# Kernel tuning notes

Measured on AMD Instinct MI355X. Metric: run time of the kernel, lower is better.

Reference implementation:

```python
import jax, jax.numpy as jnp
import numpy as np

CLP_K = 9
SCL_KS = (3, 4, 3)  # scl0_k, scl1_k, scl2_k from the source


def _ste(f, x):
    # straight-through estimator: forward f(x), identity gradient
    return x + jax.lax.stop_gradient(f(x) - x)


def floor_ste(x):
    return _ste(jnp.floor, x)


def round_ste(x):
    return _ste(jnp.round, x)


def conv_t(x, w, b):
    # torch F.conv_transpose2d with kernel 5, stride 2, padding 2, output_padding 1
    # expressed as an lhs-dilated conv; w is torch layout [in, out, kh, kw]
    k = w.shape[-1]
    wc = jnp.flip(w, axis=(-2, -1)).transpose(1, 0, 2, 3)  # -> [out, in, kh, kw]
    lo = k - 1 - 2           # k-1-padding = 2
    hi = k - 1 - 2 + 1       # + output_padding = 3
    y = jax.lax.conv_general_dilated(
        x, wc, window_strides=(1, 1), padding=[(lo, hi), (lo, hi)],
        lhs_dilation=(2, 2), dimension_numbers=('NCHW', 'OIHW', 'NCHW'))
    return y + b[None, :, None, None]


def split_deconv(x, w, b, split):
    # sum of `split` transposed convs with floor((round(W)+j)/split) quantized weights
    out = 0.0
    for j in range(split):
        wj = floor_ste((round_ste(w) + j) / split)
        bj = floor_ste((round_ste(b) + j) / split)
        out = out + conv_t(x, wj, bj)
    return out


def _g_s_forward(x, ws, bs, ms, relus, dv, Bits, split):
    # clp[i] = round((2^Bits - 1) / relus[i] * 2^(16+clp_k))
    clp = jnp.round((2.0 ** Bits - 1.0) / relus * 2.0 ** (16 + CLP_K))
    for i in range(3):
        x = split_deconv(x, ws[i], bs[i], split)
        x = x * ms[i][None, :, None, None]
        x = floor_ste((x + 2.0 ** (dv[i] - 1 - CLP_K)) / 2.0 ** (dv[i] - CLP_K))
        x = jnp.clip(x, 0.0, clp[i])
        sk = SCL_KS[i]
        scl = floor_ste((relus[i] + 2.0 ** (sk - 1)) / 2.0 ** sk)
        x = floor_ste((x * scl + 2.0 ** (15 + CLP_K - sk)) / 2.0 ** (16 + CLP_K - sk))
    x = split_deconv(x, ws[3], bs[3], split)
    x = x * ms[3][None, :, None, None]
    x = floor_ste((x + 2.0 ** (dv[3] - 9)) / 2.0 ** (dv[3] - 8))
    return x / 255.0


def setup_inputs() -> dict:
    key = jax.random.key(0)
    ks = jax.random.split(key, 16)
    N, M = 192, 320
    B, h, w = 1, 48, 48
    x = jax.random.randint(ks[0], (B, M, h, w), 0, 256).astype(jnp.float32)
    w1 = jax.random.normal(ks[1], (M, N, 5, 5), jnp.float32) * 20.0
    b1 = jax.random.normal(ks[2], (N,), jnp.float32) * 20.0
    w2 = jax.random.normal(ks[3], (N, N, 5, 5), jnp.float32) * 20.0
    b2 = jax.random.normal(ks[4], (N,), jnp.float32) * 20.0
    w3 = jax.random.normal(ks[5], (N, N, 5, 5), jnp.float32) * 20.0
    b3 = jax.random.normal(ks[6], (N,), jnp.float32) * 20.0
    w4 = jax.random.normal(ks[7], (N, 3, 5, 5), jnp.float32) * 20.0
    b4 = jax.random.normal(ks[8], (3,), jnp.float32) * 20.0
    muls0 = jax.random.randint(ks[9], (N,), 1, 1000).astype(jnp.float32)
    muls1 = jax.random.randint(ks[10], (N,), 1, 1000).astype(jnp.float32)
    muls2 = jax.random.randint(ks[11], (N,), 1, 1000).astype(jnp.float32)
    muls3 = jax.random.randint(ks[12], (3,), 1, 1000).astype(jnp.float32)
    relus = jnp.array([40000.0, 36000.0, 30000.0], jnp.float32)
    muls_dvds = jnp.array([24, 24, 24, 24], jnp.int32)
    return {"x": x, "w1": w1, "b1": b1, "w2": w2, "b2": b2, "w3": w3,
            "b3": b3, "w4": w4, "b4": b4, "muls0": muls0, "muls1": muls1,
            "muls2": muls2, "muls3": muls3, "relus": relus,
            "muls_dvds": muls_dvds, "Bits": 8, "split": 4}


def reference(x, w1, b1, w2, b2, w3, b3, w4, b4,
              muls0, muls1, muls2, muls3, relus, muls_dvds, Bits, split):
    dv = muls_dvds.astype(jnp.float32)
    ws = (w1, w2, w3, w4)
    bs = (b1, b2, b3, b4)
    ms = (muls0, muls1, muls2, muls3)
    return _g_s_forward(x, ws, bs, ms, relus, dv, int(Bits), int(split))
```

## Files before the change

### kernel.cpp

```cpp
#include <hip/hip_runtime.h>
#include <cmath>


typedef int int4v  __attribute__((ext_vector_type(4)));
typedef int int16v __attribute__((ext_vector_type(16)));

__device__ __forceinline__ void tap_to_k(int t, int& ky, int& kx) {
    if (t < 9)       { int dy = t/3,  dx = t%3;                   ky = 4-2*dy; kx = 4-2*dx; }
    else if (t < 15) { int u = t-9;   int dy = u/2, dx = 1+(u&1);  ky = 4-2*dy; kx = 5-2*dx; }
    else if (t < 21) { int u = t-15;  int dy = 1+u/3, dx = u%3;    ky = 5-2*dy; kx = 4-2*dx; }
    else             { int u = t-21;  int dy = 1+u/2, dx = 1+(u&1); ky = 5-2*dy; kx = 5-2*dx; }
}

__global__ __launch_bounds__(256)
void convert_x_t(const float* __restrict__ x, signed char* __restrict__ xh,
                 int* __restrict__ tsz, int ts_count, int C, int HW) {
    if (blockIdx.x == 0 && blockIdx.y == 0)
        for (int i = threadIdx.x; i < ts_count; i += 256) tsz[i] = 0;
    __shared__ float t[64][65];
    const int p0 = blockIdx.x * 64;
    const int c0 = blockIdx.y * 64;
    const int pL = threadIdx.x & 63;
    const int r0 = threadIdx.x >> 6;
    #pragma unroll
    for (int k = 0; k < 16; ++k) {
        int ciL = r0 * 16 + k;
        t[ciL][pL] = x[(size_t)(c0 + ciL) * HW + p0 + pL];
    }
    __syncthreads();
    #pragma unroll
    for (int k = 0; k < 16; ++k) {
        int pL2 = r0 * 16 + k;
        xh[(size_t)(p0 + pL2) * C + c0 + pL] = (signed char)((int)t[pL][pL2] - 128);
    }
}

__global__ __launch_bounds__(256)
void packA(const float* __restrict__ w1, const float* __restrict__ w2,
           const float* __restrict__ w3,
           signed char* __restrict__ p1, signed char* __restrict__ p2,
           signed char* __restrict__ p3,
           int* __restrict__ t1, int* __restrict__ t2, int* __restrict__ t3) {
    const int layer = blockIdx.y;
    const float* w = (layer == 0) ? w1 : (layer == 1) ? w2 : w3;
    signed char* out = (layer == 0) ? p1 : (layer == 1) ? p2 : p3;
    int* ts = (layer == 0) ? t1 : (layer == 1) ? t2 : t3;
    const int Cout = 192;
    const int s = blockIdx.x;
    if (layer > 0 && s >= 36) return;
    const int qs = s / 6, nb = s % 6;

    __shared__ __align__(16) signed char ls[25600];
    __shared__ int lsum[4][32];
    if (threadIdx.x < 128) ((int*)lsum)[threadIdx.x] = 0;
    __syncthreads();

    #pragma unroll
    for (int k = 0; k < 4; ++k) {
        const int pidx = threadIdx.x + k * 256;
        const int cil = pidx >> 5;
        const int col = pidx & 31;
        const int ci = qs * 32 + cil;
        const int co = nb * 32 + col;
        const float* wr = w + (size_t)(ci * Cout + co) * 25;
        const int half = cil >> 4, j = cil & 15;
        const int base = (half * 32 + col) * 16 + j;
        int psum[4] = {0, 0, 0, 0};
        #pragma unroll
        for (int t = 0; t < 25; ++t) {
            int ky, kx; tap_to_k(t, ky, kx);
            float v = rintf(wr[ky * 5 + kx]);
            v = fminf(fmaxf(v, -128.0f), 127.0f);
            int iv = (int)v;
            ls[t * 1024 + base] = (signed char)iv;
            psum[((ky & 1) << 1) | (kx & 1)] += iv;
        }
        #pragma unroll
        for (int p = 0; p < 4; ++p) atomicAdd(&lsum[p][col], psum[p]);
    }
    __syncthreads();

    signed char* dst = out + (size_t)s * 25600;
    for (int i = threadIdx.x; i < 1600; i += 256)
        *(int4v*)&dst[i * 16] = *(const int4v*)&ls[i * 16];
    if (threadIdx.x < 128) {
        const int p = threadIdx.x >> 5, col = threadIdx.x & 31;
        atomicAdd(&ts[p * Cout + nb * 32 + col], lsum[p][col]);
    }
}

__global__ void pack_w4_i8(const float* __restrict__ w, signed char* __restrict__ wpk) {
    int idx = blockIdx.x * blockDim.x + threadIdx.x;
    if (idx >= 6 * 9 * 64 * 16) return;
    int j    = idx & 15;
    int lane = (idx >> 4) & 63;
    int rem  = idx >> 10;
    int s9   = rem % 9;
    int qs   = rem / 9;
    int col  = lane & 31;
    int co   = col & 7;
    int p    = col >> 3;
    int py = p >> 1, px = p & 1;
    int dy = s9 / 3, dx = s9 % 3;
    int ci = qs * 32 + ((lane >> 5) << 4) + j;
    bool part = (py == 0 || dy >= 1) && (px == 0 || dx >= 1);
    float v = 0.0f;
    if (co < 3 && part) {
        int ky = py ? 5 - 2 * dy : 4 - 2 * dy;
        int kx = px ? 5 - 2 * dx : 4 - 2 * dx;
        v = rintf(w[(size_t)(ci * 3 + co) * 25 + ky * 5 + kx]);
        v = fminf(fmaxf(v, -128.0f), 127.0f);
    }
    wpk[idx] = (signed char)(int)v;
}

__global__ __launch_bounds__(64)
void tap_w4(const float* __restrict__ w, int* __restrict__ ts) {
    const int Cin = 192, Cout = 3;
    const int i = blockIdx.x;
    const int co = i % Cout, p = i / Cout;
    const int py = p >> 1, px = p & 1;
    const int nky = (5 - py + 1) >> 1;
    const int nkx = (5 - px + 1) >> 1;
    const int ntap = nky * nkx;
    int s = 0;
    for (int idx = threadIdx.x; idx < Cin * ntap; idx += 64) {
        const int ci = idx / ntap;
        const int u  = idx - ci * ntap;
        const int ky = py + 2 * (u / nkx);
        const int kx = px + 2 * (u % nkx);
        float v = rintf(w[(size_t)(ci * Cout + co) * 25 + ky * 5 + kx]);
        v = fminf(fmaxf(v, -128.0f), 127.0f);
        s += (int)v;
    }
    #pragma unroll
    for (int off = 32; off > 0; off >>= 1)
        s += __shfl_down(s, off, 64);
    if (threadIdx.x == 0) ts[i] = s;
}

__device__ __forceinline__ constexpr int role_nt(int role, int s9) {
    constexpr int NT0[9] = {1,1,1,1,2,2,1,2,2};
    constexpr int NT1[9] = {0,1,1,1,2,2,1,2,2};
    return role == 0 ? NT0[s9] : NT1[s9];
}
__device__ __forceinline__ constexpr int role_tap(int role, int s9, int u) {
    constexpr int T0[9][2] = {{0,0},{1,0},{2,0},{3,0},{4,21},{5,22},{6,0},{7,23},{8,24}};
    constexpr int T1[9][2] = {{0,0},{9,0},{10,0},{15,0},{11,16},{12,17},{18,0},{13,19},{14,20}};
    return role == 0 ? T0[s9][u] : T1[s9][u];
}
__device__ __forceinline__ constexpr int role_acc(int role, int s9, int u) {
    constexpr int A0[9][2] = {{0,0},{0,0},{0,0},{0,0},{0,1},{0,1},{0,0},{0,1},{0,1}};
    constexpr int A1[9][2] = {{0,0},{0,0},{0,0},{1,0},{0,1},{0,1},{1,0},{0,1},{0,1}};
    return role == 0 ? A0[s9][u] : A1[s9][u];
}

template<int ROLE, int R>
__device__ __forceinline__ void compute_role(const signed char* xs, const signed char* bs,
                                             int16v (&acc)[R][2], const int (&p0)[R],
                                             int half, int lane) {
    #pragma unroll
    for (int s9 = 0; s9 < 9; ++s9) {
        if (role_nt(ROLE, s9) == 0) continue;
        const int dy = s9 / 3, dx = s9 % 3;
        int4v a[R];
        #pragma unroll
        for (int r = 0; r < R; ++r)
            a[r] = *(const int4v*)&xs[(p0[r] + dy * 18 + dx) * 48 + half * 16];
        #pragma unroll
        for (int u = 0; u < 2; ++u) {
            if (u < role_nt(ROLE, s9)) {
                int4v b = *(const int4v*)&bs[role_tap(ROLE, s9, u) * 1024 + lane * 16];
                const int ai = role_acc(ROLE, s9, u);
                #pragma unroll
                for (int r = 0; r < R; ++r)
                    acc[r][ai] = __builtin_amdgcn_mfma_i32_32x32x32_i8(a[r], b, acc[r][ai], 0, 0, 0);
            }
        }
    }
}

template<int MW>
__global__ __launch_bounds__(MW * 64, MW == 8 ? 4 : 3)
void deconv_v8(const signed char* __restrict__ xin, const signed char* __restrict__ wpk,
               const float* __restrict__ bias, const float* __restrict__ muls,
               const int* __restrict__ tsum,
               const float* __restrict__ relus, const int* __restrict__ dvds,
               const int* __restrict__ bitsp,
               int layer, int Cin, int Cout, int NT, int Hq, int Wq,
               signed char* __restrict__ outp) {
    constexpr int R = 2;
    constexpr int PAIRS = MW / 2;
    constexpr int NROW = PAIRS * R * 2 + 2;
    constexpr int NPIX = NROW * 18;
    constexpr int THREADS = MW * 64;
    constexpr int XC = NPIX * 2;
    constexpr int XI = (XC + THREADS - 1) / THREADS;
    constexpr int BC = 1600;
    constexpr int BI = (BC + THREADS - 1) / THREADS;

    __shared__ __align__(16) signed char xs[NPIX * 48];
    __shared__ __align__(16) signed char bs[25600];

    const int tid  = threadIdx.x;
    const int lane = tid & 63;
    const int wid  = tid >> 6;
    const int pairId = wid >> 1;
    const int role   = wid & 1;
    const int qx0  = blockIdx.y * 16;
    const int qy0  = blockIdx.z * (PAIRS * R * 2);
    const int nb   = blockIdx.x;
    const int n0   = nb * 32;

    int16v acc[R][2];
    #pragma unroll
    for (int r = 0; r < R; ++r)
        #pragma unroll
        for (int p = 0; p < 2; ++p)
            #pragma unroll
            for (int e = 0; e < 16; ++e) acc[r][p][e] = 0;

    const int half   = lane >> 5;
    const int rowbit = (lane >> 4) & 1;
    const int col    = lane & 15;
    int p0[R];
    #pragma unroll
    for (int r = 0; r < R; ++r)
        p0[r] = ((pairId * R + r) * 2 + rowbit) * 18 + col;

    int4v xreg[XI], breg[BI];

    auto load_chunk = [&](int ck) {
        const signed char* wslab = wpk + (size_t)((ck >> 5) * NT + nb) * 25600;
        #pragma unroll
        for (int t = 0; t < XI; ++t) {
            int i = tid + t * THREADS;
            if (i < XC) {
                int pix = i >> 1, g = i & 1;
                int rr = pix / 18, cc = pix - rr * 18;
                int y = qy0 - 1 + rr, xx = qx0 - 1 + cc;
                int4v v = {(int)0x80808080, (int)0x80808080,
                           (int)0x80808080, (int)0x80808080};
                if ((unsigned)y < (unsigned)Hq && (unsigned)xx < (unsigned)Wq)
                    v = *(const int4v*)&xin[((size_t)y * Wq + xx) * Cin + ck + g * 16];
                xreg[t] = v;
            }
        }
        #pragma unroll
        for (int t = 0; t < BI; ++t) {
            int i = tid + t * THREADS;
            if (i < BC) breg[t] = *(const int4v*)&wslab[(size_t)i * 16];
        }
    };
    auto store_chunk = [&]() {
        #pragma unroll
        for (int t = 0; t < XI; ++t) {
            int i = tid + t * THREADS;
            if (i < XC) {
                int pix = i >> 1, g = i & 1;
                *(int4v*)&xs[pix * 48 + g * 16] = xreg[t];
            }
        }
        #pragma unroll
        for (int t = 0; t < BI; ++t) {
            int i = tid + t * THREADS;
            if (i < BC) *(int4v*)&bs[i * 16] = breg[t];
        }
    };

    load_chunk(0);
    for (int ck = 0; ck < Cin; ck += 32) {
        __syncthreads();
        store_chunk();
        __syncthreads();
        if (ck + 32 < Cin) load_chunk(ck + 32);

        if (role == 0) compute_role<0, R>(xs, bs, acc, p0, half, lane);
        else           compute_role<1, R>(xs, bs, acc, p0, half, lane);
    }

    const int dv = dvds[layer];
    float add1 = ldexpf(1.0f, dv - 10);
    float inv1 = ldexpf(1.0f, -(dv - 9));
    const float relu = relus[layer];
    const int sk = (layer == 1) ? 4 : 3;
    const float bitsv = ldexpf(1.0f, bitsp[0]) - 1.0f;
    float clp, scl;
    {
        #pragma clang fp contract(off)
        clp = rintf(bitsv / relu * 33554432.0f);
        scl = floorf((relu + ldexpf(1.0f, sk - 1)) * ldexpf(1.0f, -sk));
    }
    float add2 = ldexpf(1.0f, 24 - sk);
    float inv2 = ldexpf(1.0f, -(25 - sk));

    const int co = n0 + (lane & 31);
    float bq = rintf(bias[co]);
    float mm = muls[co];
    int pmap[2];
    pmap[0] = role == 0 ? 0 : 1;
    pmap[1] = role == 0 ? 3 : 2;
    int fullp[2];
    #pragma unroll
    for (int a = 0; a < 2; ++a) fullp[a] = tsum[pmap[a] * Cout + co];

    const int Wout = Wq * 2;

    #pragma unroll
    for (int r = 0; r < R; ++r) {
        #pragma unroll
        for (int a = 0; a < 2; ++a) {
            const int p = pmap[a];
            const int py = p >> 1, px = p & 1;
            #pragma unroll
            for (int reg = 0; reg < 16; ++reg) {
                const int mrow = (reg & 3) + 8 * (reg >> 2) + 4 * (lane >> 5);
                const int qy = qy0 + (pairId * R + r) * 2 + (mrow >> 4);
                const int qx = qx0 + (mrow & 15);
                float v = (float)(acc[r][a][reg] + 128 * fullp[a]);
                {
                    #pragma clang fp contract(off)
                    v = (v + bq) * mm;
                    v = floorf((v + add1) * inv1);
                    v = fminf(fmaxf(v, 0.0f), clp);
                    v = floorf((v * scl + add2) * inv2);
                }
                const int oy = 2 * qy + py, ox = 2 * qx + px;
                outp[((size_t)oy * Wout + ox) * Cout + co] = (signed char)((int)v - 128);
            }
        }
    }
}

__global__ __launch_bounds__(512, 4)
void deconv_final_v8(const signed char* __restrict__ xin, const signed char* __restrict__ wpk,
                     const float* __restrict__ bias, const float* __restrict__ muls,
                     const int* __restrict__ tsum, const int* __restrict__ dvds,
                     int Cin, int Hq, int Wq, float* __restrict__ outp) {
    constexpr int R = 2, MW = 8;
    constexpr int NROW = MW * R * 2 + 2;
    constexpr int NPIX = NROW * 18;
    constexpr int THREADS = 512;
    constexpr int XC = NPIX * 2;
    constexpr int XI = (XC + THREADS - 1) / THREADS;
    constexpr int BC = 576;
    constexpr int BI = (BC + THREADS - 1) / THREADS;

    __shared__ __align__(16) signed char xs[NPIX * 48];
    __shared__ __align__(16) signed char bs[9216];

    const int tid  = threadIdx.x;
    const int lane = tid & 63;
    const int wid  = tid >> 6;
    const int qx0  = blockIdx.y * 16;
    const int qy0  = blockIdx.z * (MW * R * 2);

    int16v acc[R];
    #pragma unroll
    for (int r = 0; r < R; ++r)
        #pragma unroll
        for (int e = 0; e < 16; ++e) acc[r][e] = 0;

    const int half   = lane >> 5;
    const int rowbit = (lane >> 4) & 1;
    const int col    = lane & 15;
    int p0[R];
    #pragma unroll
    for (int r = 0; r < R; ++r)
        p0[r] = ((wid * R + r) * 2 + rowbit) * 18 + col;

    int4v xreg[XI], breg[BI];

    auto load_chunk = [&](int ck) {
        const signed char* wslab = wpk + (size_t)(ck >> 5) * 9216;
        #pragma unroll
        for (int t = 0; t < XI; ++t) {
            int i = tid + t * THREADS;
            if (i < XC) {
                int pix = i >> 1, g = i & 1;
                int rr = pix / 18, cc = pix - rr * 18;
                int y = qy0 - 1 + rr, xx = qx0 - 1 + cc;
                int4v v = {(int)0x80808080, (int)0x80808080,
                           (int)0x80808080, (int)0x80808080};
                if ((unsigned)y < (unsigned)Hq && (unsigned)xx < (unsigned)Wq)
                    v = *(const int4v*)&xin[((size_t)y * Wq + xx) * Cin + ck + g * 16];
                xreg[t] = v;
            }
        }
        #pragma unroll
        for (int t = 0; t < BI; ++t) {
            int i = tid + t * THREADS;
            if (i < BC) breg[t] = *(const int4v*)&wslab[(size_t)i * 16];
        }
    };
    auto store_chunk = [&]() {
        #pragma unroll
        for (int t = 0; t < XI; ++t) {
            int i = tid + t * THREADS;
            if (i < XC) {
                int pix = i >> 1, g = i & 1;
                *(int4v*)&xs[pix * 48 + g * 16] = xreg[t];
            }
        }
        #pragma unroll
        for (int t = 0; t < BI; ++t) {
            int i = tid + t * THREADS;
            if (i < BC) *(int4v*)&bs[i * 16] = breg[t];
        }
    };

    load_chunk(0);
    for (int ck = 0; ck < Cin; ck += 32) {
        __syncthreads();
        store_chunk();
        __syncthreads();
        if (ck + 32 < Cin) load_chunk(ck + 32);

        #pragma unroll
        for (int s9 = 0; s9 < 9; ++s9) {
            const int dy = s9 / 3, dx = s9 % 3;
            int4v b = *(const int4v*)&bs[s9 * 1024 + lane * 16];
            #pragma unroll
            for (int r = 0; r < R; ++r) {
                int4v a = *(const int4v*)&xs[(p0[r] + dy * 18 + dx) * 48 + half * 16];
                acc[r] = __builtin_amdgcn_mfma_i32_32x32x32_i8(a, b, acc[r], 0, 0, 0);
            }
        }
    }

    const int dv = dvds[3];
    const float add1 = ldexpf(1.0f, dv - 9);
    const float inv1 = ldexpf(1.0f, -(dv - 8));

    const int coln = lane & 31;
    const int co = coln & 7;
    const int p  = coln >> 3;
    const int py = p >> 1, px = p & 1;
    const bool valid = (co < 3);
    float bq = 0.f, mm = 0.f;
    int fp = 0;
    if (valid) { bq = rintf(bias[co]); mm = muls[co]; fp = tsum[p * 3 + co]; }

    const int Wout = Wq * 2, Hout = Hq * 2;
    #pragma unroll
    for (int r = 0; r < R; ++r) {
        #pragma unroll
        for (int reg = 0; reg < 16; ++reg) {
            const int mrow = (reg & 3) + 8 * (reg >> 2) + 4 * (lane >> 5);
            const int qy = qy0 + (wid * R + r) * 2 + (mrow >> 4);
            const int qx = qx0 + (mrow & 15);
            float v = (float)(acc[r][reg] + 128 * fp);
            {
                #pragma clang fp contract(off)
                v = (v + bq) * mm;
                v = floorf((v + add1) * inv1);
                v = v / 255.0f;
            }
            if (valid) {
                const int oy = 2 * qy + py, ox = 2 * qx + px;
                outp[((size_t)co * Hout + oy) * Wout + ox] = v;
            }
        }
    }
}

extern "C" void kernel_launch(void* const* d_in, const int* in_sizes, int n_in,
                              void* d_out, int out_size, void* d_ws, size_t ws_size,
                              hipStream_t stream) {
    const float* x  = (const float*)d_in[0];
    const float* w1 = (const float*)d_in[1];
    const float* b1 = (const float*)d_in[2];
    const float* w2 = (const float*)d_in[3];
    const float* b2 = (const float*)d_in[4];
    const float* w3 = (const float*)d_in[5];
    const float* b3 = (const float*)d_in[6];
    const float* w4 = (const float*)d_in[7];
    const float* b4 = (const float*)d_in[8];
    const float* m0 = (const float*)d_in[9];
    const float* m1 = (const float*)d_in[10];
    const float* m2 = (const float*)d_in[11];
    const float* m3 = (const float*)d_in[12];
    const float* relus = (const float*)d_in[13];
    const int* dvds = (const int*)d_in[14];
    const int* bitsp = (const int*)d_in[15];

    signed char* wsb = (signed char*)d_ws;
    size_t o = 0;
    signed char* wpk1 = wsb + o; o += (size_t)10 * 6 * 25600;
    signed char* wpk2 = wsb + o; o += (size_t)6 * 6 * 25600;
    signed char* wpk3 = wsb + o; o += (size_t)6 * 6 * 25600;
    signed char* wpk4 = wsb + o; o += (size_t)6 * 9216;
    int* ts1 = (int*)(wsb + o); o += 4 * 192 * 4;
    int* ts2 = (int*)(wsb + o); o += 4 * 192 * 4;
    int* ts3 = (int*)(wsb + o); o += 4 * 192 * 4;
    int* ts4 = (int*)(wsb + o); o += 4 * 4 * 4;
    o = (o + 15) & ~(size_t)15;
    signed char* xh = wsb + o; o += (size_t)48 * 48 * 320;
    signed char* a1 = wsb + o; o += (size_t)96 * 96 * 192;
    signed char* a2 = wsb + o; o += (size_t)192 * 192 * 192;
    signed char* a3 = wsb + o; o += (size_t)384 * 384 * 192;

    const int ts_count = 4 * 192 * 3 + 4 * 4;

    convert_x_t<<<dim3(36, 5), 256, 0, stream>>>(x, xh, ts1, ts_count, 320, 48 * 48);
    packA<<<dim3(60, 3), 256, 0, stream>>>(w1, w2, w3, wpk1, wpk2, wpk3, ts1, ts2, ts3);
    pack_w4_i8<<<(6 * 9 * 1024 + 255) / 256, 256, 0, stream>>>(w4, wpk4);
    tap_w4<<<12, 64, 0, stream>>>(w4, ts4);

    deconv_v8<4><<<dim3(6, 3, 6), 256, 0, stream>>>(
        xh, wpk1, b1, m0, ts1, relus, dvds, bitsp, 0, 320, 192, 6, 48, 48, a1);
    deconv_v8<8><<<dim3(6, 6, 6), 512, 0, stream>>>(
        a1, wpk2, b2, m1, ts2, relus, dvds, bitsp, 1, 192, 192, 6, 96, 96, a2);
    deconv_v8<8><<<dim3(6, 12, 12), 512, 0, stream>>>(
        a2, wpk3, b3, m2, ts3, relus, dvds, bitsp, 2, 192, 192, 6, 192, 192, a3);
    deconv_final_v8<<<dim3(1, 24, 12), 512, 0, stream>>>(
        a3, wpk4, b4, m3, ts4, dvds, 192, 384, 384, (float*)d_out);
}
```

Measured before the change: 213.3 us.

## Read weights directly from global memory and double-buffer input tiles in LDS

Weight tiles are no longer staged through shared memory. Each wave reads its MFMA B operands straight from the packed weight slab in global memory, which should be served by the cache. The input halo tile is double-buffered in LDS, so each chunk needs one barrier instead of two, and the per-thread global addresses are precomputed once. Blocks shrink to 4 waves with more blocks in the grid, which cuts LDS use and may raise occupancy. The cost is repeated global or L2 weight loads on the MFMA critical path.

```diff
diff --git a/kernel.cpp b/kernel.cpp
--- a/kernel.cpp
+++ b/kernel.cpp
@@ -156,7 +156,8 @@
 }
 
 template<int ROLE, int R>
-__device__ __forceinline__ void compute_role(const signed char* xs, const signed char* bs,
+__device__ __forceinline__ void compute_role(const signed char* xsb,
+                                             const signed char* __restrict__ wslab,
                                              int16v (&acc)[R][2], const int (&p0)[R],
                                              int half, int lane) {
     #pragma unroll
@@ -166,11 +167,11 @@
         int4v a[R];
         #pragma unroll
         for (int r = 0; r < R; ++r)
-            a[r] = *(const int4v*)&xs[(p0[r] + dy * 18 + dx) * 48 + half * 16];
+            a[r] = *(const int4v*)&xsb[(p0[r] + dy * 18 + dx) * 48 + half * 16];
         #pragma unroll
         for (int u = 0; u < 2; ++u) {
             if (u < role_nt(ROLE, s9)) {
-                int4v b = *(const int4v*)&bs[role_tap(ROLE, s9, u) * 1024 + lane * 16];
+                int4v b = *(const int4v*)&wslab[role_tap(ROLE, s9, u) * 1024 + lane * 16];
                 const int ai = role_acc(ROLE, s9, u);
                 #pragma unroll
                 for (int r = 0; r < R; ++r)
@@ -180,27 +181,23 @@
     }
 }
 
-template<int MW>
-__global__ __launch_bounds__(MW * 64, MW == 8 ? 4 : 3)
-void deconv_v8(const signed char* __restrict__ xin, const signed char* __restrict__ wpk,
+template<int MW, int R>
+__global__ __launch_bounds__(MW * 64, 4)
+void deconv_v9(const signed char* __restrict__ xin, const signed char* __restrict__ wpk,
                const float* __restrict__ bias, const float* __restrict__ muls,
                const int* __restrict__ tsum,
                const float* __restrict__ relus, const int* __restrict__ dvds,
                const int* __restrict__ bitsp,
                int layer, int Cin, int Cout, int NT, int Hq, int Wq,
                signed char* __restrict__ outp) {
-    constexpr int R = 2;
     constexpr int PAIRS = MW / 2;
     constexpr int NROW = PAIRS * R * 2 + 2;
     constexpr int NPIX = NROW * 18;
     constexpr int THREADS = MW * 64;
     constexpr int XC = NPIX * 2;
     constexpr int XI = (XC + THREADS - 1) / THREADS;
-    constexpr int BC = 1600;
-    constexpr int BI = (BC + THREADS - 1) / THREADS;
-
-    __shared__ __align__(16) signed char xs[NPIX * 48];
-    __shared__ __align__(16) signed char bs[25600];
+
+    __shared__ __align__(16) signed char xs[2][NPIX * 48];
 
     const int tid  = threadIdx.x;
     const int lane = tid & 63;
@@ -228,55 +225,53 @@
     for (int r = 0; r < R; ++r)
         p0[r] = ((pairId * R + r) * 2 + rowbit) * 18 + col;
 
-    int4v xreg[XI], breg[BI];
-
-    auto load_chunk = [&](int ck) {
-        const signed char* wslab = wpk + (size_t)((ck >> 5) * NT + nb) * 25600;
+    const signed char* xptr[XI];
+    int  xsoff[XI];
+    bool xok[XI];
+    #pragma unroll
+    for (int t = 0; t < XI; ++t) {
+        int i = tid + t * THREADS;
+        xok[t] = false; xsoff[t] = 0; xptr[t] = xin;
+        if (i < XC) {
+            int pix = i >> 1, g = i & 1;
+            int rr = pix / 18, cc = pix - rr * 18;
+            int y = qy0 - 1 + rr, xx = qx0 - 1 + cc;
+            xsoff[t] = pix * 48 + g * 16;
+            xok[t] = (unsigned)y < (unsigned)Hq && (unsigned)xx < (unsigned)Wq;
+            if (xok[t]) xptr[t] = xin + ((size_t)y * Wq + xx) * Cin + g * 16;
+        }
+    }
+
+    int4v xreg[XI];
+    auto load_x = [&](int ck) {
         #pragma unroll
         for (int t = 0; t < XI; ++t) {
             int i = tid + t * THREADS;
             if (i < XC) {
-                int pix = i >> 1, g = i & 1;
-                int rr = pix / 18, cc = pix - rr * 18;
-                int y = qy0 - 1 + rr, xx = qx0 - 1 + cc;
                 int4v v = {(int)0x80808080, (int)0x80808080,
                            (int)0x80808080, (int)0x80808080};
-                if ((unsigned)y < (unsigned)Hq && (unsigned)xx < (unsigned)Wq)
-                    v = *(const int4v*)&xin[((size_t)y * Wq + xx) * Cin + ck + g * 16];
+                if (xok[t]) v = *(const int4v*)(xptr[t] + ck);
                 xreg[t] = v;
             }
         }
-        #pragma unroll
-        for (int t = 0; t < BI; ++t) {
-            int i = tid + t * THREADS;
-            if (i < BC) breg[t] = *(const int4v*)&wslab[(size_t)i * 16];
-        }
     };
-    auto store_chunk = [&]() {
+    auto store_x = [&](int buf) {
         #pragma unroll
         for (int t = 0; t < XI; ++t) {
             int i = tid + t * THREADS;
-            if (i < XC) {
-                int pix = i >> 1, g = i & 1;
-                *(int4v*)&xs[pix * 48 + g * 16] = xreg[t];
-            }
-        }
-        #pragma unroll
-        for (int t = 0; t < BI; ++t) {
-            int i = tid + t * THREADS;
-            if (i < BC) *(int4v*)&bs[i * 16] = breg[t];
+            if (i < XC) *(int4v*)&xs[buf][xsoff[t]] = xreg[t];
         }
     };
 
-    load_chunk(0);
-    for (int ck = 0; ck < Cin; ck += 32) {
+    load_x(0);
+    int buf = 0;
+    for (int ck = 0; ck < Cin; ck += 32, buf ^= 1) {
+        store_x(buf);
         __syncthreads();
-        store_chunk();
-        __syncthreads();
-        if (ck + 32 < Cin) load_chunk(ck + 32);
-
-        if (role == 0) compute_role<0, R>(xs, bs, acc, p0, half, lane);
-        else           compute_role<1, R>(xs, bs, acc, p0, half, lane);
+        if (ck + 32 < Cin) load_x(ck + 32);
+        const signed char* wslab = wpk + (size_t)((ck >> 5) * NT + nb) * 25600;
+        if (role == 0) compute_role<0, R>(xs[buf], wslab, acc, p0, half, lane);
+        else           compute_role<1, R>(xs[buf], wslab, acc, p0, half, lane);
     }
 
     const int dv = dvds[layer];
@@ -332,22 +327,19 @@
     }
 }
 
-__global__ __launch_bounds__(512, 4)
-void deconv_final_v8(const signed char* __restrict__ xin, const signed char* __restrict__ wpk,
+__global__ __launch_bounds__(256, 4)
+void deconv_final_v9(const signed char* __restrict__ xin, const signed char* __restrict__ wpk,
                      const float* __restrict__ bias, const float* __restrict__ muls,
                      const int* __restrict__ tsum, const int* __restrict__ dvds,
                      int Cin, int Hq, int Wq, float* __restrict__ outp) {
-    constexpr int R = 2, MW = 8;
+    constexpr int R = 2, MW = 4;
     constexpr int NROW = MW * R * 2 + 2;
     constexpr int NPIX = NROW * 18;
-    constexpr int THREADS = 512;
+    constexpr int THREADS = 256;
     constexpr int XC = NPIX * 2;
     constexpr int XI = (XC + THREADS - 1) / THREADS;
-    constexpr int BC = 576;
-    constexpr int BI = (BC + THREADS - 1) / THREADS;
-
-    __shared__ __align__(16) signed char xs[NPIX * 48];
-    __shared__ __align__(16) signed char bs[9216];
+
+    __shared__ __align__(16) signed char xs[2][NPIX * 48];
 
     const int tid  = threadIdx.x;
     const int lane = tid & 63;
@@ -369,60 +361,59 @@
     for (int r = 0; r < R; ++r)
         p0[r] = ((wid * R + r) * 2 + rowbit) * 18 + col;
 
-    int4v xreg[XI], breg[BI];
-
-    auto load_chunk = [&](int ck) {
-        const signed char* wslab = wpk + (size_t)(ck >> 5) * 9216;
+    const signed char* xptr[XI];
+    int  xsoff[XI];
+    bool xok[XI];
+    #pragma unroll
+    for (int t = 0; t < XI; ++t) {
+        int i = tid + t * THREADS;
+        xok[t] = false; xsoff[t] = 0; xptr[t] = xin;
+        if (i < XC) {
+            int pix = i >> 1, g = i & 1;
+            int rr = pix / 18, cc = pix - rr * 18;
+            int y = qy0 - 1 + rr, xx = qx0 - 1 + cc;
+            xsoff[t] = pix * 48 + g * 16;
+            xok[t] = (unsigned)y < (unsigned)Hq && (unsigned)xx < (unsigned)Wq;
+            if (xok[t]) xptr[t] = xin + ((size_t)y * Wq + xx) * Cin + g * 16;
+        }
+    }
+
+    int4v xreg[XI];
+    auto load_x = [&](int ck) {
         #pragma unroll
         for (int t = 0; t < XI; ++t) {
             int i = tid + t * THREADS;
             if (i < XC) {
-                int pix = i >> 1, g = i & 1;
-                int rr = pix / 18, cc = pix - rr * 18;
-                int y = qy0 - 1 + rr, xx = qx0 - 1 + cc;
                 int4v v = {(int)0x80808080, (int)0x80808080,
                            (int)0x80808080, (int)0x80808080};
-                if ((unsigned)y < (unsigned)Hq && (unsigned)xx < (unsigned)Wq)
-                    v = *(const int4v*)&xin[((size_t)y * Wq + xx) * Cin + ck + g * 16];
+                if (xok[t]) v = *(const int4v*)(xptr[t] + ck);
                 xreg[t] = v;
             }
         }
-        #pragma unroll
-        for (int t = 0; t < BI; ++t) {
-            int i = tid + t * THREADS;
-            if (i < BC) breg[t] = *(const int4v*)&wslab[(size_t)i * 16];
-        }
     };
-    auto store_chunk = [&]() {
+    auto store_x = [&](int buf) {
         #pragma unroll
         for (int t = 0; t < XI; ++t) {
             int i = tid + t * THREADS;
-            if (i < XC) {
-                int pix = i >> 1, g = i & 1;
-                *(int4v*)&xs[pix * 48 + g * 16] = xreg[t];
-            }
-        }
-        #pragma unroll
-        for (int t = 0; t < BI; ++t) {
-            int i = tid + t * THREADS;
-            if (i < BC) *(int4v*)&bs[i * 16] = breg[t];
+            if (i < XC) *(int4v*)&xs[buf][xsoff[t]] = xreg[t];
         }
     };
 
-    load_chunk(0);
-    for (int ck = 0; ck < Cin; ck += 32) {
+    load_x(0);
+    int buf = 0;
+    for (int ck = 0; ck < Cin; ck += 32, buf ^= 1) {
+        store_x(buf);
         __syncthreads();
-        store_chunk();
-        __syncthreads();
-        if (ck + 32 < Cin) load_chunk(ck + 32);
+        if (ck + 32 < Cin) load_x(ck + 32);
+        const signed char* wslab = wpk + (size_t)(ck >> 5) * 9216;
 
         #pragma unroll
         for (int s9 = 0; s9 < 9; ++s9) {
             const int dy = s9 / 3, dx = s9 % 3;
-            int4v b = *(const int4v*)&bs[s9 * 1024 + lane * 16];
+            int4v b = *(const int4v*)&wslab[s9 * 1024 + lane * 16];
             #pragma unroll
             for (int r = 0; r < R; ++r) {
-                int4v a = *(const int4v*)&xs[(p0[r] + dy * 18 + dx) * 48 + half * 16];
+                int4v a = *(const int4v*)&xs[buf][(p0[r] + dy * 18 + dx) * 48 + half * 16];
                 acc[r] = __builtin_amdgcn_mfma_i32_32x32x32_i8(a, b, acc[r], 0, 0, 0);
             }
         }
@@ -507,12 +498,12 @@
     pack_w4_i8<<<(6 * 9 * 1024 + 255) / 256, 256, 0, stream>>>(w4, wpk4);
     tap_w4<<<12, 64, 0, stream>>>(w4, ts4);
 
-    deconv_v8<4><<<dim3(6, 3, 6), 256, 0, stream>>>(
+    deconv_v9<4, 2><<<dim3(6, 3, 6), 256, 0, stream>>>(
         xh, wpk1, b1, m0, ts1, relus, dvds, bitsp, 0, 320, 192, 6, 48, 48, a1);
-    deconv_v8<8><<<dim3(6, 6, 6), 512, 0, stream>>>(
+    deconv_v9<4, 2><<<dim3(6, 6, 12), 256, 0, stream>>>(
         a1, wpk2, b2, m1, ts2, relus, dvds, bitsp, 1, 192, 192, 6, 96, 96, a2);
-    deconv_v8<8><<<dim3(6, 12, 12), 512, 0, stream>>>(
+    deconv_v9<4, 2><<<dim3(6, 12, 24), 256, 0, stream>>>(
         a2, wpk3, b3, m2, ts3, relus, dvds, bitsp, 2, 192, 192, 6, 192, 192, a3);
-    deconv_final_v8<<<dim3(1, 24, 12), 512, 0, stream>>>(
+    deconv_final_v9<<<dim3(1, 24, 24), 256, 0, stream>>>(
         a3, wpk4, b4, m3, ts4, dvds, 192, 384, 384, (float*)d_out);
 }
```

After: 263.0 us. +23.3%, slower.

## Double-buffer weight tiles via async global-to-LDS DMA and remap blocks per XCD

Applied to the files above, without the earlier changes.

Weight slabs are now copied straight from global memory into LDS with global_load_lds instead of passing through registers, into a double-buffered LDS array, so the next chunk's weights load while the current chunk is computed. Activations still go through registers. The 3D grid becomes a 1D grid with explicit decoding. For layer 3, consecutive spatial tiles are grouped onto the same XCD to improve L2 locality. LDS use per block roughly doubles, which may cut the number of resident blocks per CU.

```diff
diff --git a/kernel.cpp b/kernel.cpp
--- a/kernel.cpp
+++ b/kernel.cpp
@@ -4,6 +4,14 @@
 
 typedef int int4v  __attribute__((ext_vector_type(4)));
 typedef int int16v __attribute__((ext_vector_type(16)));
+
+#define GLOBAL_AS __attribute__((address_space(1)))
+#define LDS_AS    __attribute__((address_space(3)))
+
+__device__ __forceinline__ void dma16(const signed char* g, signed char* l) {
+    __builtin_amdgcn_global_load_lds((const GLOBAL_AS int*)g, (LDS_AS int*)l,
+                                     16, 0, 0);
+}
 
 __device__ __forceinline__ void tap_to_k(int t, int& ky, int& kx) {
     if (t < 9)       { int dy = t/3,  dx = t%3;                   ky = 4-2*dy; kx = 4-2*dx; }
@@ -156,7 +164,7 @@
 }
 
 template<int ROLE, int R>
-__device__ __forceinline__ void compute_role(const signed char* xs, const signed char* bs,
+__device__ __forceinline__ void compute_role(const signed char* xsb, const signed char* bsb,
                                              int16v (&acc)[R][2], const int (&p0)[R],
                                              int half, int lane) {
     #pragma unroll
@@ -166,11 +174,11 @@
         int4v a[R];
         #pragma unroll
         for (int r = 0; r < R; ++r)
-            a[r] = *(const int4v*)&xs[(p0[r] + dy * 18 + dx) * 48 + half * 16];
+            a[r] = *(const int4v*)&xsb[(p0[r] + dy * 18 + dx) * 48 + half * 16];
         #pragma unroll
         for (int u = 0; u < 2; ++u) {
             if (u < role_nt(ROLE, s9)) {
-                int4v b = *(const int4v*)&bs[role_tap(ROLE, s9, u) * 1024 + lane * 16];
+                int4v b = *(const int4v*)&bsb[role_tap(ROLE, s9, u) * 1024 + lane * 16];
                 const int ai = role_acc(ROLE, s9, u);
                 #pragma unroll
                 for (int r = 0; r < R; ++r)
@@ -180,16 +188,16 @@
     }
 }
 
-template<int MW>
+template<int MW, int R>
 __global__ __launch_bounds__(MW * 64, MW == 8 ? 4 : 3)
-void deconv_v8(const signed char* __restrict__ xin, const signed char* __restrict__ wpk,
-               const float* __restrict__ bias, const float* __restrict__ muls,
-               const int* __restrict__ tsum,
-               const float* __restrict__ relus, const int* __restrict__ dvds,
-               const int* __restrict__ bitsp,
-               int layer, int Cin, int Cout, int NT, int Hq, int Wq,
-               signed char* __restrict__ outp) {
-    constexpr int R = 2;
+void deconv_v11(const signed char* __restrict__ xin, const signed char* __restrict__ wpk,
+                const float* __restrict__ bias, const float* __restrict__ muls,
+                const int* __restrict__ tsum,
+                const float* __restrict__ relus, const int* __restrict__ dvds,
+                const int* __restrict__ bitsp,
+                int layer, int Cin, int Cout, int NT, int Hq, int Wq,
+                int NB, int NQX, int T8,
+                signed char* __restrict__ outp) {
     constexpr int PAIRS = MW / 2;
     constexpr int NROW = PAIRS * R * 2 + 2;
     constexpr int NPIX = NROW * 18;
@@ -197,20 +205,34 @@
     constexpr int XC = NPIX * 2;
     constexpr int XI = (XC + THREADS - 1) / THREADS;
     constexpr int BC = 1600;
-    constexpr int BI = (BC + THREADS - 1) / THREADS;
+    constexpr int BTI = (BC + THREADS - 1) / THREADS;
 
     __shared__ __align__(16) signed char xs[NPIX * 48];
-    __shared__ __align__(16) signed char bs[25600];
+    __shared__ __align__(16) signed char bs[2][25600];
 
     const int tid  = threadIdx.x;
     const int lane = tid & 63;
     const int wid  = tid >> 6;
     const int pairId = wid >> 1;
     const int role   = wid & 1;
-    const int qx0  = blockIdx.y * 16;
-    const int qy0  = blockIdx.z * (PAIRS * R * 2);
-    const int nb   = blockIdx.x;
-    const int n0   = nb * 32;
+
+    int nb, qx, qy;
+    {
+        const int bi = blockIdx.x;
+        if (T8 > 0) {
+            const int xcd = bi & 7, j = bi >> 3;
+            const int tl = j / NB, n = j - tl * NB;
+            const int tile = xcd * T8 + tl;
+            nb = n; qx = tile % NQX; qy = tile / NQX;
+        } else {
+            nb = bi % NB;
+            const int s = bi / NB;
+            qx = s % NQX; qy = s / NQX;
+        }
+    }
+    const int qx0 = qx * 16;
+    const int qy0 = qy * (PAIRS * R * 2);
+    const int n0  = nb * 32;
 
     int16v acc[R][2];
     #pragma unroll
@@ -228,10 +250,8 @@
     for (int r = 0; r < R; ++r)
         p0[r] = ((pairId * R + r) * 2 + rowbit) * 18 + col;
 
-    int4v xreg[XI], breg[BI];
-
-    auto load_chunk = [&](int ck) {
-        const signed char* wslab = wpk + (size_t)((ck >> 5) * NT + nb) * 25600;
+    int4v xreg[XI];
+    auto load_x = [&](int ck) {
         #pragma unroll
         for (int t = 0; t < XI; ++t) {
             int i = tid + t * THREADS;
@@ -246,13 +266,8 @@
                 xreg[t] = v;
             }
         }
-        #pragma unroll
-        for (int t = 0; t < BI; ++t) {
-            int i = tid + t * THREADS;
-            if (i < BC) breg[t] = *(const int4v*)&wslab[(size_t)i * 16];
-        }
     };
-    auto store_chunk = [&]() {
+    auto store_x = [&]() {
         #pragma unroll
         for (int t = 0; t < XI; ++t) {
             int i = tid + t * THREADS;
@@ -261,22 +276,29 @@
                 *(int4v*)&xs[pix * 48 + g * 16] = xreg[t];
             }
         }
-        #pragma unroll
-        for (int t = 0; t < BI; ++t) {
+    };
+    auto dma_b = [&](const signed char* wslab, signed char* dst) {
+        #pragma unroll
+        for (int t = 0; t < BTI; ++t) {
             int i = tid + t * THREADS;
-            if (i < BC) *(int4v*)&bs[i * 16] = breg[t];
+            if (i < BC)
+                dma16(wslab + (size_t)i * 16, dst + (size_t)i * 16);
         }
     };
 
-    load_chunk(0);
+    load_x(0);
+    dma_b(wpk + (size_t)nb * 25600, bs[0]);
     for (int ck = 0; ck < Cin; ck += 32) {
+        const int cbuf = (ck >> 5) & 1;
         __syncthreads();
-        store_chunk();
+        store_x();
         __syncthreads();
-        if (ck + 32 < Cin) load_chunk(ck + 32);
-
-        if (role == 0) compute_role<0, R>(xs, bs, acc, p0, half, lane);
-        else           compute_role<1, R>(xs, bs, acc, p0, half, lane);
+        if (ck + 32 < Cin) {
+            load_x(ck + 32);
+            dma_b(wpk + (size_t)(((ck >> 5) + 1) * NT + nb) * 25600, bs[cbuf ^ 1]);
+        }
+        if (role == 0) compute_role<0, R>(xs, bs[cbuf], acc, p0, half, lane);
+        else           compute_role<1, R>(xs, bs[cbuf], acc, p0, half, lane);
     }
 
     const int dv = dvds[layer];
@@ -315,8 +337,8 @@
             #pragma unroll
             for (int reg = 0; reg < 16; ++reg) {
                 const int mrow = (reg & 3) + 8 * (reg >> 2) + 4 * (lane >> 5);
-                const int qy = qy0 + (pairId * R + r) * 2 + (mrow >> 4);
-                const int qx = qx0 + (mrow & 15);
+                const int qy2 = qy0 + (pairId * R + r) * 2 + (mrow >> 4);
+                const int qx2 = qx0 + (mrow & 15);
                 float v = (float)(acc[r][a][reg] + 128 * fullp[a]);
                 {
                     #pragma clang fp contract(off)
@@ -325,7 +347,7 @@
                     v = fminf(fmaxf(v, 0.0f), clp);
                     v = floorf((v * scl + add2) * inv2);
                 }
-                const int oy = 2 * qy + py, ox = 2 * qx + px;
+                const int oy = 2 * qy2 + py, ox = 2 * qx2 + px;
                 outp[((size_t)oy * Wout + ox) * Cout + co] = (signed char)((int)v - 128);
             }
         }
@@ -333,10 +355,10 @@
 }
 
 __global__ __launch_bounds__(512, 4)
-void deconv_final_v8(const signed char* __restrict__ xin, const signed char* __restrict__ wpk,
-                     const float* __restrict__ bias, const float* __restrict__ muls,
-                     const int* __restrict__ tsum, const int* __restrict__ dvds,
-                     int Cin, int Hq, int Wq, float* __restrict__ outp) {
+void deconv_final_v11(const signed char* __restrict__ xin, const signed char* __restrict__ wpk,
+                      const float* __restrict__ bias, const float* __restrict__ muls,
+                      const int* __restrict__ tsum, const int* __restrict__ dvds,
+                      int Cin, int Hq, int Wq, float* __restrict__ outp) {
     constexpr int R = 2, MW = 8;
     constexpr int NROW = MW * R * 2 + 2;
     constexpr int NPIX = NROW * 18;
@@ -344,10 +366,10 @@
     constexpr int XC = NPIX * 2;
     constexpr int XI = (XC + THREADS - 1) / THREADS;
     constexpr int BC = 576;
-    constexpr int BI = (BC + THREADS - 1) / THREADS;
+    constexpr int BTI = (BC + THREADS - 1) / THREADS;
 
     __shared__ __align__(16) signed char xs[NPIX * 48];
-    __shared__ __align__(16) signed char bs[9216];
+    __shared__ __align__(16) signed char bs[2][9216];
 
     const int tid  = threadIdx.x;
     const int lane = tid & 63;
@@ -369,10 +391,8 @@
     for (int r = 0; r < R; ++r)
         p0[r] = ((wid * R + r) * 2 + rowbit) * 18 + col;
 
-    int4v xreg[XI], breg[BI];
-
-    auto load_chunk = [&](int ck) {
-        const signed char* wslab = wpk + (size_t)(ck >> 5) * 9216;
+    int4v xreg[XI];
+    auto load_x = [&](int ck) {
         #pragma unroll
         for (int t = 0; t < XI; ++t) {
             int i = tid + t * THREADS;
@@ -387,13 +407,8 @@
                 xreg[t] = v;
             }
         }
-        #pragma unroll
-        for (int t = 0; t < BI; ++t) {
-            int i = tid + t * THREADS;
-            if (i < BC) breg[t] = *(const int4v*)&wslab[(size_t)i * 16];
-        }
     };
-    auto store_chunk = [&]() {
+    auto store_x = [&]() {
         #pragma unroll
         for (int t = 0; t < XI; ++t) {
             int i = tid + t * THREADS;
@@ -402,24 +417,32 @@
                 *(int4v*)&xs[pix * 48 + g * 16] = xreg[t];
             }
         }
-        #pragma unroll
-        for (int t = 0; t < BI; ++t) {
+    };
+    auto dma_b = [&](const signed char* wslab, signed char* dst) {
+        #pragma unroll
+        for (int t = 0; t < BTI; ++t) {
             int i = tid + t * THREADS;
-            if (i < BC) *(int4v*)&bs[i * 16] = breg[t];
+            if (i < BC)
+                dma16(wslab + (size_t)i * 16, dst + (size_t)i * 16);
         }
     };
 
-    load_chunk(0);
+    load_x(0);
+    dma_b(wpk, bs[0]);
     for (int ck = 0; ck < Cin; ck += 32) {
+        const int cbuf = (ck >> 5) & 1;
         __syncthreads();
-        store_chunk();
+        store_x();
         __syncthreads();
-        if (ck + 32 < Cin) load_chunk(ck + 32);
+        if (ck + 32 < Cin) {
+            load_x(ck + 32);
+            dma_b(wpk + (size_t)((ck >> 5) + 1) * 9216, bs[cbuf ^ 1]);
+        }
 
         #pragma unroll
         for (int s9 = 0; s9 < 9; ++s9) {
             const int dy = s9 / 3, dx = s9 % 3;
-            int4v b = *(const int4v*)&bs[s9 * 1024 + lane * 16];
+            int4v b = *(const int4v*)&bs[cbuf][s9 * 1024 + lane * 16];
             #pragma unroll
             for (int r = 0; r < R; ++r) {
                 int4v a = *(const int4v*)&xs[(p0[r] + dy * 18 + dx) * 48 + half * 16];
@@ -507,12 +530,15 @@
     pack_w4_i8<<<(6 * 9 * 1024 + 255) / 256, 256, 0, stream>>>(w4, wpk4);
     tap_w4<<<12, 64, 0, stream>>>(w4, ts4);
 
-    deconv_v8<4><<<dim3(6, 3, 6), 256, 0, stream>>>(
-        xh, wpk1, b1, m0, ts1, relus, dvds, bitsp, 0, 320, 192, 6, 48, 48, a1);
-    deconv_v8<8><<<dim3(6, 6, 6), 512, 0, stream>>>(
-        a1, wpk2, b2, m1, ts2, relus, dvds, bitsp, 1, 192, 192, 6, 96, 96, a2);
-    deconv_v8<8><<<dim3(6, 12, 12), 512, 0, stream>>>(
-        a2, wpk3, b3, m2, ts3, relus, dvds, bitsp, 2, 192, 192, 6, 192, 192, a3);
-    deconv_final_v8<<<dim3(1, 24, 12), 512, 0, stream>>>(
+    deconv_v11<4, 2><<<108, 256, 0, stream>>>(
+        xh, wpk1, b1, m0, ts1, relus, dvds, bitsp, 0, 320, 192, 6, 48, 48,
+        6, 3, 0, a1);
+    deconv_v11<8, 2><<<216, 512, 0, stream>>>(
+        a1, wpk2, b2, m1, ts2, relus, dvds, bitsp, 1, 192, 192, 6, 96, 96,
+        6, 6, 0, a2);
+    deconv_v11<8, 2><<<864, 512, 0, stream>>>(
+        a2, wpk3, b3, m2, ts3, relus, dvds, bitsp, 2, 192, 192, 6, 192, 192,
+        6, 12, 18, a3);
+    deconv_final_v11<<<dim3(1, 24, 12), 512, 0, stream>>>(
         a3, wpk4, b4, m3, ts4, dvds, 192, 384, 384, (float*)d_out);
 }
```

After: 212.9 us. Within noise of the previous version (-0.2%).
